# Kernel tuning notes

Hardware: AMD Instinct MI355X
Metric: run time of the kernel (lower is better)

The kernel has to match this reference:

```python
import jax, jax.numpy as jnp
import numpy as np

B, C, L = 64, 64, 8192
EPS = float(np.finfo(np.float32).eps)  # matches np.finfo(np.float32).eps in the torch code


def setup_inputs() -> dict:
    key = jax.random.key(0)
    k1, k2, k3 = jax.random.split(key, 3)
    data = jax.random.normal(k1, (B, C, L), dtype=jnp.float32)
    idxes = jax.random.randint(k2, (B, L), 0, L).astype(jnp.int32)
    # prefix lengths in [1, L] so every slice is non-empty (ragged branch)
    zero_pos = jax.random.randint(k3, (B,), 1, L + 1)
    return {"data": data, "idxes": idxes, "zero_pos": zero_pos}


def reference(data, idxes, zero_pos):
    # data: [B, C, L]; per-batch mean/std over the prefix data[b, :, :zero_pos[b]]
    Bn, Cn, Ln = data.shape
    mask = (jnp.arange(Ln)[None, :] < zero_pos[:, None])[:, None, :].astype(data.dtype)  # [B,1,L]
    cnt = Cn * zero_pos.astype(data.dtype)  # [B] number of elements in each prefix
    mean = jnp.sum(data * mask, axis=(1, 2)) / cnt  # [B]
    diff = (data - mean[:, None, None]) * mask  # [B,C,L]
    var = jnp.sum(diff * diff, axis=(1, 2)) / (cnt - 1.0)  # unbiased, as torch.std
    std = jnp.sqrt(var)  # [B]
    out = (data - mean[:, None, None]) / (std[:, None, None] + EPS)
    return (out, idxes, zero_pos)
```

## Files before the change

### kernel.cpp

```cpp
#include <hip/hip_runtime.h>
#include <math.h>

#define BB 64
#define CC 64
#define LL 8192
#define EPS_F 1.1920928955078125e-07f

#define NB_STAT (BB * CC)
#define NB_AUX  512
#define ROW4 (LL / 4)

#define NB_NORM 8192

typedef float f4 __attribute__((ext_vector_type(4)));
typedef int   i4 __attribute__((ext_vector_type(4)));


__global__ __launch_bounds__(256) void tln_stats(const float* __restrict__ data,
                          const int* __restrict__ zero_pos,
                          const i4* __restrict__ idxes,
                          float2* __restrict__ partials,
                          f4* __restrict__ out_idx,
                          float* __restrict__ out_zp) {
    const int blk = blockIdx.x;
    const int tid = threadIdx.x;

    if (blk < NB_STAT) {
        const int b = blk >> 6;
        const int c = blk & 63;
        const int zp = zero_pos[b];
        const int nv = zp >> 2;
        const float* rowp = data + ((size_t)b * CC + c) * LL;
        const f4* p = (const f4*)rowp;

        float s0 = 0.f, s1 = 0.f, s2 = 0.f, s3 = 0.f;
        float q0 = 0.f, q1 = 0.f, q2 = 0.f, q3 = 0.f;
        int i = tid;
        for (; i + 768 < nv; i += 1024) {
            f4 a = p[i], d = p[i + 256], e = p[i + 512], g = p[i + 768];
            s0 += a.x+a.y+a.z+a.w;  q0 += a.x*a.x+a.y*a.y+a.z*a.z+a.w*a.w;
            s1 += d.x+d.y+d.z+d.w;  q1 += d.x*d.x+d.y*d.y+d.z*d.z+d.w*d.w;
            s2 += e.x+e.y+e.z+e.w;  q2 += e.x*e.x+e.y*e.y+e.z*e.z+e.w*e.w;
            s3 += g.x+g.y+g.z+g.w;  q3 += g.x*g.x+g.y*g.y+g.z*g.z+g.w*g.w;
        }
        for (; i < nv; i += 256) {
            f4 a = p[i];
            s0 += a.x+a.y+a.z+a.w;  q0 += a.x*a.x+a.y*a.y+a.z*a.z+a.w*a.w;
        }
        {
            const int l = (nv << 2) + tid;
            if (l < zp) {
                float v = rowp[l];
                s0 += v; q0 += v * v;
            }
        }
        float sum = (s0 + s1) + (s2 + s3);
        float sq  = (q0 + q1) + (q2 + q3);

        #pragma unroll
        for (int off = 32; off > 0; off >>= 1) {
            sum += __shfl_down(sum, off);
            sq  += __shfl_down(sq, off);
        }
        __shared__ float lsum[4], lsq[4];
        const int wave = tid >> 6;
        const int lane = tid & 63;
        if (lane == 0) { lsum[wave] = sum; lsq[wave] = sq; }
        __syncthreads();
        if (tid == 0) {
            float2 pr;
            pr.x = lsum[0] + lsum[1] + lsum[2] + lsum[3];
            pr.y = lsq[0] + lsq[1] + lsq[2] + lsq[3];
            partials[blk] = pr;
        }
    } else {
        const int j = blk - NB_STAT;
        const int ii = j * 256 + tid;
        i4 v = idxes[ii];
        f4 o = __builtin_convertvector(v, f4);
        __builtin_nontemporal_store(o, out_idx + ii);
        if (j == 0 && tid < BB) out_zp[tid] = (float)zero_pos[tid];
    }
}

__global__ __launch_bounds__(256) void tln_fused(const f4* __restrict__ data4,
                          const float2* __restrict__ partials,
                          const int* __restrict__ zero_pos,
                          f4* __restrict__ out4) {
    const int blk = blockIdx.x;
    const int tid = threadIdx.x;
    const int b = blk >> 7;
    const int t = blk & 127;
    const int lane = tid & 63;

    float2 p = partials[(b << 6) + lane];
    float s_ = p.x, q_ = p.y;
    #pragma unroll
    for (int off = 32; off > 0; off >>= 1) {
        s_ += __shfl_xor(s_, off);
        q_ += __shfl_xor(q_, off);
    }
    const float cnt  = (float)CC * (float)zero_pos[b];
    const float mean = s_ / cnt;
    const float var  = (q_ - cnt * mean * mean) / (cnt - 1.0f);
    const float inv  = 1.0f / (sqrtf(var) + EPS_F);

    const size_t base = ((size_t)b << 17) | ((size_t)t << 10) | (size_t)tid;
    f4 cur = data4[base];
    #pragma unroll
    for (int k = 0; k < 3; ++k) {
        f4 nxt = data4[base + (size_t)((k + 1) << 8)];
        __builtin_nontemporal_store((cur - mean) * inv,
                                    out4 + base + (size_t)(k << 8));
        cur = nxt;
    }
    __builtin_nontemporal_store((cur - mean) * inv, out4 + base + (size_t)(3 << 8));
}

extern "C" void kernel_launch(void* const* d_in, const int* in_sizes, int n_in,
                              void* d_out, int out_size, void* d_ws, size_t ws_size,
                              hipStream_t stream) {
    const float* data    = (const float*)d_in[0];
    const int* idxes     = (const int*)d_in[1];
    const int* zero_pos  = (const int*)d_in[2];

    float2* partials = (float2*)d_ws;

    float* out_data = (float*)d_out;
    float* out_idx  = out_data + (size_t)BB * CC * LL;
    float* out_zp   = out_idx + (size_t)BB * LL;

    tln_stats<<<NB_STAT + NB_AUX, 256, 0, stream>>>(
        data, zero_pos, (const i4*)idxes, partials, (f4*)out_idx, out_zp);

    tln_fused<<<NB_NORM, 256, 0, stream>>>(
        (const f4*)data, partials, zero_pos, (f4*)out_data);
}
```

Measured before the change: 241.4 us.

## Read full rows with masked accumulation and hoist data loads before stats reduction

The stats kernel no longer uses a prefix-length-dependent loop. It always issues eight fixed vector loads per thread covering the whole row and masks elements at or beyond zero_pos to zero. This evens out work across blocks and makes all loads independent and issued together, at the cost of reading the masked tail that the old loop skipped. The normalize kernel now issues all four data loads before the partials reduction, so memory latency overlaps the shuffle-based mean/std computation.

```diff
diff --git a/kernel.cpp b/kernel.cpp
--- a/kernel.cpp
+++ b/kernel.cpp
@@ -16,6 +16,15 @@
 typedef int   i4 __attribute__((ext_vector_type(4)));
 
 
+#define ACC(v, l0, sacc, qacc) do {                       \
+    float x0 = ((l0) + 0 < zp) ? (v).x : 0.0f;            \
+    float x1 = ((l0) + 1 < zp) ? (v).y : 0.0f;            \
+    float x2 = ((l0) + 2 < zp) ? (v).z : 0.0f;            \
+    float x3 = ((l0) + 3 < zp) ? (v).w : 0.0f;            \
+    sacc += (x0 + x1) + (x2 + x3);                        \
+    qacc += (x0*x0 + x1*x1) + (x2*x2 + x3*x3);            \
+} while (0)
+
 __global__ __launch_bounds__(256) void tln_stats(const float* __restrict__ data,
                           const int* __restrict__ zero_pos,
                           const i4* __restrict__ idxes,
@@ -27,32 +36,23 @@
 
     if (blk < NB_STAT) {
         const int b = blk >> 6;
-        const int c = blk & 63;
         const int zp = zero_pos[b];
-        const int nv = zp >> 2;
-        const float* rowp = data + ((size_t)b * CC + c) * LL;
-        const f4* p = (const f4*)rowp;
+        const f4* p = (const f4*)(data + (size_t)blk * LL);
 
         float s0 = 0.f, s1 = 0.f, s2 = 0.f, s3 = 0.f;
         float q0 = 0.f, q1 = 0.f, q2 = 0.f, q3 = 0.f;
-        int i = tid;
-        for (; i + 768 < nv; i += 1024) {
-            f4 a = p[i], d = p[i + 256], e = p[i + 512], g = p[i + 768];
-            s0 += a.x+a.y+a.z+a.w;  q0 += a.x*a.x+a.y*a.y+a.z*a.z+a.w*a.w;
-            s1 += d.x+d.y+d.z+d.w;  q1 += d.x*d.x+d.y*d.y+d.z*d.z+d.w*d.w;
-            s2 += e.x+e.y+e.z+e.w;  q2 += e.x*e.x+e.y*e.y+e.z*e.z+e.w*e.w;
-            s3 += g.x+g.y+g.z+g.w;  q3 += g.x*g.x+g.y*g.y+g.z*g.z+g.w*g.w;
-        }
-        for (; i < nv; i += 256) {
+        #pragma unroll
+        for (int w = 0; w < 2; ++w) {
+            const int i = (w << 10) + tid;
             f4 a = p[i];
-            s0 += a.x+a.y+a.z+a.w;  q0 += a.x*a.x+a.y*a.y+a.z*a.z+a.w*a.w;
-        }
-        {
-            const int l = (nv << 2) + tid;
-            if (l < zp) {
-                float v = rowp[l];
-                s0 += v; q0 += v * v;
-            }
+            f4 d = p[i + 256];
+            f4 e = p[i + 512];
+            f4 g = p[i + 768];
+            const int l = i << 2;
+            ACC(a, l,        s0, q0);
+            ACC(d, l + 1024, s1, q1);
+            ACC(e, l + 2048, s2, q2);
+            ACC(g, l + 3072, s3, q3);
         }
         float sum = (s0 + s1) + (s2 + s3);
         float sq  = (q0 + q1) + (q2 + q3);
@@ -90,8 +90,13 @@
     const int blk = blockIdx.x;
     const int tid = threadIdx.x;
     const int b = blk >> 7;
-    const int t = blk & 127;
     const int lane = tid & 63;
+
+    const size_t base = (size_t)blk * 1024 + tid;
+    f4 v0 = data4[base];
+    f4 v1 = data4[base + 256];
+    f4 v2 = data4[base + 512];
+    f4 v3 = data4[base + 768];
 
     float2 p = partials[(b << 6) + lane];
     float s_ = p.x, q_ = p.y;
@@ -105,16 +110,10 @@
     const float var  = (q_ - cnt * mean * mean) / (cnt - 1.0f);
     const float inv  = 1.0f / (sqrtf(var) + EPS_F);
 
-    const size_t base = ((size_t)b << 17) | ((size_t)t << 10) | (size_t)tid;
-    f4 cur = data4[base];
-    #pragma unroll
-    for (int k = 0; k < 3; ++k) {
-        f4 nxt = data4[base + (size_t)((k + 1) << 8)];
-        __builtin_nontemporal_store((cur - mean) * inv,
-                                    out4 + base + (size_t)(k << 8));
-        cur = nxt;
-    }
-    __builtin_nontemporal_store((cur - mean) * inv, out4 + base + (size_t)(3 << 8));
+    __builtin_nontemporal_store((v0 - mean) * inv, out4 + base);
+    __builtin_nontemporal_store((v1 - mean) * inv, out4 + base + 256);
+    __builtin_nontemporal_store((v2 - mean) * inv, out4 + base + 512);
+    __builtin_nontemporal_store((v3 - mean) * inv, out4 + base + 768);
 }
 
 extern "C" void kernel_launch(void* const* d_in, const int* in_sizes, int n_in,
```

Measured after the change: 251.4 us. 1.04x slower.
